# Performance work log

Measured on AMD Instinct MI355X. Metric: run time of the kernel, lower is better.

Reference implementation:

```python
import jax, jax.numpy as jnp
import numpy as np


def conv1x1(x, w, b):
    # x: [B,Cin,H,W], w: [Cout,Cin], b: [Cout]
    return jnp.einsum('bchw,oc->bohw', x, w) + b[None, :, None, None]


def setup_inputs() -> dict:
    key = jax.random.key(0)
    ks = jax.random.split(key, 10)
    B, Cm, C, H, W = 4, 6, 64, 64, 64
    map1 = jax.random.normal(ks[0], (B, Cm, H, W), jnp.float32)
    map2 = jax.random.normal(ks[1], (B, Cm, H, W), jnp.float32)
    feature_map = jax.random.normal(ks[2], (B, C, H, W), jnp.float32)
    # 1x1 conv params (kaiming-ish scale)
    wb = jax.random.normal(ks[3], (Cm, Cm), jnp.float32) / np.sqrt(Cm)
    bb = jnp.zeros((Cm,), jnp.float32)
    wc = jax.random.normal(ks[4], (Cm, Cm), jnp.float32) / np.sqrt(Cm)
    bc = jnp.zeros((Cm,), jnp.float32)
    wd = jax.random.normal(ks[5], (C, C), jnp.float32) / np.sqrt(C)
    bd = jnp.zeros((C,), jnp.float32)
    alpha = jnp.zeros((1,), jnp.float32)
    return {"map1": map1, "map2": map2, "feature_map": feature_map,
            "wb": wb, "bb": bb, "wc": wc, "bc": bc, "wd": wd, "bd": bd,
            "alpha": alpha}


def reference(map1, map2, feature_map, wb, bb, wc, bc, wd, bd, alpha):
    B, _, H, W = map1.shape
    N = H * W
    # conv1x1 projections, flatten spatial
    feat_b = conv1x1(map1, wb, bb).reshape(B, -1, N).transpose(0, 2, 1)  # [B,N,6]
    feat_c = conv1x1(map2, wc, bc).reshape(B, -1, N)                      # [B,6,N]
    attention_s = jax.nn.softmax(jnp.einsum('bnc,bcm->bnm', feat_b, feat_c), axis=-1)  # [B,N,N]
    feat_d = conv1x1(feature_map, wd, bd).reshape(B, -1, N)               # [B,C,N]
    # bmm with attention_s^T: out[b,c,n] = sum_m feat_d[b,c,m] * attn[b,n,m]
    feat_e = jnp.einsum('bcm,bnm->bcn', feat_d, attention_s).reshape(B, -1, H, W)
    return alpha * feat_e + feature_map
```

## Files before the change

kernel.cpp:

```cpp
#include <hip/hip_runtime.h>
#include <hip/hip_bf16.h>
#include <math.h>


#define BATCH 4
#define CMAP  6
#define CH    64
#define NSP   4096
#define TN    64
#define NTH   32
#define PSTR  72

typedef __attribute__((ext_vector_type(8))) short short8;
typedef __attribute__((ext_vector_type(4))) float f32x4;

#if __has_builtin(__builtin_amdgcn_exp2f)
#define EXP2(x) __builtin_amdgcn_exp2f(x)
#else
#define EXP2(x) exp2f(x)
#endif

__device__ __forceinline__ unsigned f2bf(float f) {
    unsigned u = __float_as_uint(f);
    return (u + 0x7fffu + ((u >> 16) & 1u)) >> 16;
}

#define INVLN2 1.44269504088896f
#define SHIFT_BF16 0xC238u
#define ONE_BF16   0x3F80u


__global__ void proj_kernel(const float* __restrict__ map1, const float* __restrict__ map2,
                            const float* __restrict__ fm,
                            const float* __restrict__ wb, const float* __restrict__ bb,
                            const float* __restrict__ wc, const float* __restrict__ bc,
                            const float* __restrict__ wd, const float* __restrict__ bd,
                            unsigned short* __restrict__ featq8,
                            unsigned short* __restrict__ featk8,
                            unsigned short* __restrict__ featdf)
{
    __shared__ unsigned short vfrag[2048];

    const int b    = blockIdx.z;
    const int half = blockIdx.y;
    const int lane = threadIdx.x & 63;
    const int og   = threadIdx.x >> 6;
    const int n    = blockIdx.x * 64 + lane;

    const int ht = lane >> 5;
    const int mm = lane & 31;
    const int q4 = mm >> 3, jj = mm & 7;
    const int cb_local = og >> 1;
    float vals[CH];
#pragma unroll
    for (int c = 0; c < CH; ++c)
        vals[c] = fm[(size_t)(b*CH + c)*NSP + n];
#pragma unroll
    for (int oi = 0; oi < 8; ++oi) {
        const int o = half*32 + og*8 + oi;
        float a = bd[o];
#pragma unroll
        for (int c = 0; c < CH; ++c)
            a = fmaf(vals[c], wd[o*CH + c], a);
        const int r = (og & 1)*8 + oi;
        vfrag[(ht*2 + cb_local)*512 + (q4*16 + r)*8 + jj] = (unsigned short)f2bf(a);
    }

    if (half == 0 && og == 0) {
        float v1[CMAP], v2[CMAP];
#pragma unroll
        for (int c = 0; c < CMAP; ++c) {
            v1[c] = map1[(size_t)(b*CMAP + c)*NSP + n];
            v2[c] = map2[(size_t)(b*CMAP + c)*NSP + n];
        }
        unsigned qv[CMAP], kv[CMAP];
#pragma unroll
        for (int o = 0; o < CMAP; ++o) {
            float a1 = bb[o], a2 = bc[o];
#pragma unroll
            for (int c = 0; c < CMAP; ++c) {
                a1 = fmaf(v1[c], wb[o*CMAP + c], a1);
                a2 = fmaf(v2[c], wc[o*CMAP + c], a2);
            }
            qv[o] = f2bf(a1 * INVLN2);
            kv[o] = f2bf(a2);
        }
        uint4 qw, kw;
        qw.x = qv[0] | (qv[1] << 16);
        qw.y = qv[2] | (qv[3] << 16);
        qw.z = qv[4] | (qv[5] << 16);
        qw.w = SHIFT_BF16;
        kw.x = kv[0] | (kv[1] << 16);
        kw.y = kv[2] | (kv[3] << 16);
        kw.z = kv[4] | (kv[5] << 16);
        kw.w = ONE_BF16;
        *(uint4*)&featq8[(size_t)(b*NSP + n)*8] = qw;
        *(uint4*)&featk8[(size_t)(b*NSP + n)*8] = kw;
    }

    __syncthreads();

    {
        const int tt = threadIdx.x;
        const uint4 d = *(const uint4*)&vfrag[tt*8];
        const int ht2 = tt >> 7, inner = tt & 127;
        const size_t off = (((size_t)(b*128 + blockIdx.x*2 + ht2)*4) + half*2)*512
                         + (size_t)inner*8;
        *(uint4*)&featdf[off] = d;
    }
}

__global__ __launch_bounds__(256, 4)
void attn_kernel(const unsigned short* __restrict__ featq8,
                 const unsigned short* __restrict__ featk8,
                 const unsigned short* __restrict__ featdf,
                 const float* __restrict__ fm, const float* __restrict__ alpha_p,
                 float* __restrict__ out)
{
    __shared__ unsigned short p_scr[2][4][16*PSTR];
    __shared__ float cmb[2][64][20];

    const int b    = blockIdx.z;
    const int chh  = blockIdx.y;
    const int t    = threadIdx.x;
    const int lane = t & 63, w = t >> 6;
    const int row16 = lane & 15, quad = lane >> 4;
    const int qsub  = w >> 1;
    const int khalf = w & 1;
    const int n0w  = blockIdx.x * 32 + qsub * 16;
    const int m0   = khalf * (NSP/2);

    short8 qf = {0,0,0,0,0,0,0,0};
    if (quad == 0)
        qf = *(const short8*)&featq8[(size_t)(b*NSP + n0w + row16)*8];

    const short8 onesb = {(short)ONE_BF16,(short)ONE_BF16,(short)ONE_BF16,(short)ONE_BF16,
                          (short)ONE_BF16,(short)ONE_BF16,(short)ONE_BF16,(short)ONE_BF16};

    const unsigned short* kbase = featk8 + ((size_t)(b*NSP + m0) + row16)*8 + quad*8;
    const unsigned short* vfb = featdf + ((size_t)b*128*4)*512 + lane*8;
    const int hb  = khalf * 64;
    const int cb0 = chh*2, cb1 = chh*2 + 1;

    const f32x4 zf = {0.f,0.f,0.f,0.f};
    f32x4 acc[2] = {zf, zf};
    f32x4 accL = zf;
    const int prow = row16 * PSTR;

#define PAM_DO(pwp, mb, sv)                                                     \
    {                                                                           \
        const float p0 = EXP2(sv[0]), p1 = EXP2(sv[1]);                         \
        const float p2 = EXP2(sv[2]), p3 = EXP2(sv[3]);                         \
        uint2 pp;                                                               \
        pp.x = __builtin_amdgcn_perm(__float_as_uint(p1), __float_as_uint(p0), 0x07060302u); \
        pp.y = __builtin_amdgcn_perm(__float_as_uint(p3), __float_as_uint(p2), 0x07060302u); \
        *(uint2*)((pwp) + (mb)*16) = pp;                                        \
    }

#define LOADK(mt)                                                               \
    kc0 = *(const short8*)(kbase + ((mt)*TN +  0)*8);                           \
    kc1 = *(const short8*)(kbase + ((mt)*TN + 16)*8);                           \
    kc2 = *(const short8*)(kbase + ((mt)*TN + 32)*8);                           \
    kc3 = *(const short8*)(kbase + ((mt)*TN + 48)*8);

#define LOADV(vt)                                                               \
    vv0 = *(const short8*)(vfb + (size_t)((hb + (vt)*2 + 0)*4 + cb0)*512);      \
    vv1 = *(const short8*)(vfb + (size_t)((hb + (vt)*2 + 1)*4 + cb0)*512);      \
    vv2 = *(const short8*)(vfb + (size_t)((hb + (vt)*2 + 0)*4 + cb1)*512);      \
    vv3 = *(const short8*)(vfb + (size_t)((hb + (vt)*2 + 1)*4 + cb1)*512);

#define PV(a0_, a1_)                                                            \
    acc[0] = __builtin_amdgcn_mfma_f32_16x16x32_bf16(a0_, vv0, acc[0], 0, 0, 0); \
    acc[0] = __builtin_amdgcn_mfma_f32_16x16x32_bf16(a1_, vv1, acc[0], 0, 0, 0); \
    acc[1] = __builtin_amdgcn_mfma_f32_16x16x32_bf16(a0_, vv2, acc[1], 0, 0, 0); \
    acc[1] = __builtin_amdgcn_mfma_f32_16x16x32_bf16(a1_, vv3, acc[1], 0, 0, 0); \
    accL   = __builtin_amdgcn_mfma_f32_16x16x32_bf16(a0_, onesb, accL, 0, 0, 0); \
    accL   = __builtin_amdgcn_mfma_f32_16x16x32_bf16(a1_, onesb, accL, 0, 0, 0);

    short8 kc0, kc1, kc2, kc3;
    short8 vv0, vv1, vv2, vv3;
    f32x4 sp0, sp1, sp2, sp3;

    LOADK(0)
    {
        f32x4 a0 = __builtin_amdgcn_mfma_f32_16x16x32_bf16(kc0, qf, zf, 0, 0, 0);
        f32x4 a1 = __builtin_amdgcn_mfma_f32_16x16x32_bf16(kc1, qf, zf, 0, 0, 0);
        f32x4 a2 = __builtin_amdgcn_mfma_f32_16x16x32_bf16(kc2, qf, zf, 0, 0, 0);
        f32x4 a3 = __builtin_amdgcn_mfma_f32_16x16x32_bf16(kc3, qf, zf, 0, 0, 0);
        LOADK(1)
        unsigned short* pw = &p_scr[0][w][prow + quad*4];
        PAM_DO(pw, 0, a0) PAM_DO(pw, 1, a1) PAM_DO(pw, 2, a2) PAM_DO(pw, 3, a3)
    }
    sp0 = __builtin_amdgcn_mfma_f32_16x16x32_bf16(kc0, qf, zf, 0, 0, 0);
    sp1 = __builtin_amdgcn_mfma_f32_16x16x32_bf16(kc1, qf, zf, 0, 0, 0);
    sp2 = __builtin_amdgcn_mfma_f32_16x16x32_bf16(kc2, qf, zf, 0, 0, 0);
    sp3 = __builtin_amdgcn_mfma_f32_16x16x32_bf16(kc3, qf, zf, 0, 0, 0);
    LOADK(2)
    LOADV(0)

#pragma unroll 2
    for (int i = 2; i < NTH; ++i) {
        const f32x4 t0 = __builtin_amdgcn_mfma_f32_16x16x32_bf16(kc0, qf, zf, 0, 0, 0);
        const f32x4 t1 = __builtin_amdgcn_mfma_f32_16x16x32_bf16(kc1, qf, zf, 0, 0, 0);
        const f32x4 t2 = __builtin_amdgcn_mfma_f32_16x16x32_bf16(kc2, qf, zf, 0, 0, 0);
        const f32x4 t3 = __builtin_amdgcn_mfma_f32_16x16x32_bf16(kc3, qf, zf, 0, 0, 0);

        LOADK(i + 1)

        const unsigned short* pr = &p_scr[i & 1][w][prow + quad*8];
        const short8 a0 = *(const short8*)pr;
        const short8 a1 = *(const short8*)(pr + 32);

        {
            unsigned short* pw = &p_scr[(i + 1) & 1][w][prow + quad*4];
            PAM_DO(pw, 0, sp0) PAM_DO(pw, 1, sp1) PAM_DO(pw, 2, sp2) PAM_DO(pw, 3, sp3)
        }

        PV(a0, a1)

        LOADV(i - 1)

        sp0 = t0; sp1 = t1; sp2 = t2; sp3 = t3;
    }

    {
        const unsigned short* pr = &p_scr[0][w][prow + quad*8];
        const short8 a0 = *(const short8*)pr;
        const short8 a1 = *(const short8*)(pr + 32);
        unsigned short* pw = &p_scr[1][w][prow + quad*4];
        PAM_DO(pw, 0, sp0) PAM_DO(pw, 1, sp1) PAM_DO(pw, 2, sp2) PAM_DO(pw, 3, sp3)
        PV(a0, a1)
        LOADV(31)
    }
    {
        const unsigned short* pr = &p_scr[1][w][prow + quad*8];
        const short8 a0 = *(const short8*)pr;
        const short8 a1 = *(const short8*)(pr + 32);
        PV(a0, a1)
    }
#undef PAM_DO
#undef LOADK
#undef LOADV
#undef PV

    if (khalf == 1) {
        float* c = cmb[qsub][lane];
#pragma unroll
        for (int cb = 0; cb < 2; ++cb)
            *(float4*)&c[cb*4] = (float4){acc[cb][0], acc[cb][1], acc[cb][2], acc[cb][3]};
        *(float4*)&c[16] = (float4){accL[0], accL[1], accL[2], accL[3]};
    }
    __syncthreads();
    if (khalf == 0) {
        const float* c = cmb[qsub][lane];
        const float4 lo = *(const float4*)&c[16];
        const float alpha = alpha_p[0];
        const float c0 = alpha / (accL[0] + lo.x + 1e-30f);
        const float c1 = alpha / (accL[1] + lo.y + 1e-30f);
        const float c2 = alpha / (accL[2] + lo.z + 1e-30f);
        const float c3 = alpha / (accL[3] + lo.w + 1e-30f);
#pragma unroll
        for (int cb = 0; cb < 2; ++cb) {
            const float4 po = *(const float4*)&c[cb*4];
            const int ch = chh*32 + cb*16 + row16;
            const size_t base = (size_t)(b*CH + ch)*NSP + n0w + quad*4;
            const float4 f = *(const float4*)&fm[base];
            float4 o;
            o.x = fmaf(c0, acc[cb][0] + po.x, f.x);
            o.y = fmaf(c1, acc[cb][1] + po.y, f.y);
            o.z = fmaf(c2, acc[cb][2] + po.z, f.z);
            o.w = fmaf(c3, acc[cb][3] + po.w, f.w);
            *(float4*)&out[base] = o;
        }
    }
}

extern "C" void kernel_launch(void* const* d_in, const int* in_sizes, int n_in,
                              void* d_out, int out_size, void* d_ws, size_t ws_size,
                              hipStream_t stream)
{
    const float* map1  = (const float*)d_in[0];
    const float* map2  = (const float*)d_in[1];
    const float* fm    = (const float*)d_in[2];
    const float* wb    = (const float*)d_in[3];
    const float* bb    = (const float*)d_in[4];
    const float* wc    = (const float*)d_in[5];
    const float* bc    = (const float*)d_in[6];
    const float* wd    = (const float*)d_in[7];
    const float* bd    = (const float*)d_in[8];
    const float* alpha = (const float*)d_in[9];
    float* out = (float*)d_out;

    unsigned short* featq8 = (unsigned short*)d_ws;
    unsigned short* featk8 = featq8 + (size_t)BATCH*NSP*8;
    unsigned short* featdf = featk8 + (size_t)BATCH*NSP*8;

    proj_kernel<<<dim3(NSP/64, 2, BATCH), 256, 0, stream>>>(
        map1, map2, fm, wb, bb, wc, bc, wd, bd, featq8, featk8, featdf);
    attn_kernel<<<dim3(NSP/32, 2, BATCH), 256, 0, stream>>>(
        featq8, featk8, featdf, fm, alpha, out);
}
```

Baseline: 123.9 us.

## Keep softmax probabilities in registers and compute all 64 channels per block

The attention kernel now computes the transposed score tile, with K rows permuted so that the MFMA output layout matches the B-operand layout of the P·V MFMA. Exponentiated scores are packed straight into registers, which removes the LDS write/read round trip of the probability scratch. Each block now handles all 64 output channels instead of splitting channels across two blocks, so the QK and exp work is no longer duplicated. The cost is more registers (launch bounds drop to 2 blocks per CU), half as many blocks, and scalar rather than vectorised output stores.

```diff
diff --git a/kernel.cpp b/kernel.cpp
--- a/kernel.cpp
+++ b/kernel.cpp
@@ -9,7 +9,6 @@
 #define NSP   4096
 #define TN    64
 #define NTH   32
-#define PSTR  72
 
 typedef __attribute__((ext_vector_type(8))) short short8;
 typedef __attribute__((ext_vector_type(4))) float f32x4;
@@ -110,18 +109,16 @@
     }
 }
 
-__global__ __launch_bounds__(256, 4)
+__global__ __launch_bounds__(256, 2)
 void attn_kernel(const unsigned short* __restrict__ featq8,
                  const unsigned short* __restrict__ featk8,
                  const unsigned short* __restrict__ featdf,
                  const float* __restrict__ fm, const float* __restrict__ alpha_p,
                  float* __restrict__ out)
 {
-    __shared__ unsigned short p_scr[2][4][16*PSTR];
     __shared__ float cmb[2][64][20];
 
-    const int b    = blockIdx.z;
-    const int chh  = blockIdx.y;
+    const int b    = blockIdx.y;
     const int t    = threadIdx.x;
     const int lane = t & 63, w = t >> 6;
     const int row16 = lane & 15, quad = lane >> 4;
@@ -134,143 +131,128 @@
     if (quad == 0)
         qf = *(const short8*)&featq8[(size_t)(b*NSP + n0w + row16)*8];
 
-    const short8 onesb = {(short)ONE_BF16,(short)ONE_BF16,(short)ONE_BF16,(short)ONE_BF16,
+    const short8 onesA = {(short)ONE_BF16,(short)ONE_BF16,(short)ONE_BF16,(short)ONE_BF16,
                           (short)ONE_BF16,(short)ONE_BF16,(short)ONE_BF16,(short)ONE_BF16};
 
-    const unsigned short* kbase = featk8 + ((size_t)(b*NSP + m0) + row16)*8 + quad*8;
+    const int perm16 = ((row16 >> 2) << 3) + (row16 & 3);
+    const unsigned short* kbase = featk8 + ((size_t)(b*NSP + m0) + perm16)*8 + quad*8;
     const unsigned short* vfb = featdf + ((size_t)b*128*4)*512 + lane*8;
-    const int hb  = khalf * 64;
-    const int cb0 = chh*2, cb1 = chh*2 + 1;
+    const int hb = khalf * 64;
 
     const f32x4 zf = {0.f,0.f,0.f,0.f};
-    f32x4 acc[2] = {zf, zf};
+    f32x4 acc[4] = {zf, zf, zf, zf};
     f32x4 accL = zf;
-    const int prow = row16 * PSTR;
-
-#define PAM_DO(pwp, mb, sv)                                                     \
-    {                                                                           \
-        const float p0 = EXP2(sv[0]), p1 = EXP2(sv[1]);                         \
-        const float p2 = EXP2(sv[2]), p3 = EXP2(sv[3]);                         \
-        uint2 pp;                                                               \
-        pp.x = __builtin_amdgcn_perm(__float_as_uint(p1), __float_as_uint(p0), 0x07060302u); \
-        pp.y = __builtin_amdgcn_perm(__float_as_uint(p3), __float_as_uint(p2), 0x07060302u); \
-        *(uint2*)((pwp) + (mb)*16) = pp;                                        \
-    }
 
 #define LOADK(mt)                                                               \
     kc0 = *(const short8*)(kbase + ((mt)*TN +  0)*8);                           \
-    kc1 = *(const short8*)(kbase + ((mt)*TN + 16)*8);                           \
+    kc1 = *(const short8*)(kbase + ((mt)*TN +  4)*8);                           \
     kc2 = *(const short8*)(kbase + ((mt)*TN + 32)*8);                           \
-    kc3 = *(const short8*)(kbase + ((mt)*TN + 48)*8);
+    kc3 = *(const short8*)(kbase + ((mt)*TN + 36)*8);
 
 #define LOADV(vt)                                                               \
-    vv0 = *(const short8*)(vfb + (size_t)((hb + (vt)*2 + 0)*4 + cb0)*512);      \
-    vv1 = *(const short8*)(vfb + (size_t)((hb + (vt)*2 + 1)*4 + cb0)*512);      \
-    vv2 = *(const short8*)(vfb + (size_t)((hb + (vt)*2 + 0)*4 + cb1)*512);      \
-    vv3 = *(const short8*)(vfb + (size_t)((hb + (vt)*2 + 1)*4 + cb1)*512);
-
-#define PV(a0_, a1_)                                                            \
-    acc[0] = __builtin_amdgcn_mfma_f32_16x16x32_bf16(a0_, vv0, acc[0], 0, 0, 0); \
-    acc[0] = __builtin_amdgcn_mfma_f32_16x16x32_bf16(a1_, vv1, acc[0], 0, 0, 0); \
-    acc[1] = __builtin_amdgcn_mfma_f32_16x16x32_bf16(a0_, vv2, acc[1], 0, 0, 0); \
-    acc[1] = __builtin_amdgcn_mfma_f32_16x16x32_bf16(a1_, vv3, acc[1], 0, 0, 0); \
-    accL   = __builtin_amdgcn_mfma_f32_16x16x32_bf16(a0_, onesb, accL, 0, 0, 0); \
-    accL   = __builtin_amdgcn_mfma_f32_16x16x32_bf16(a1_, onesb, accL, 0, 0, 0);
+    vv0 = *(const short8*)(vfb + (size_t)((hb + (vt)*2 + 0)*4 + 0)*512);        \
+    vv1 = *(const short8*)(vfb + (size_t)((hb + (vt)*2 + 1)*4 + 0)*512);        \
+    vv2 = *(const short8*)(vfb + (size_t)((hb + (vt)*2 + 0)*4 + 1)*512);        \
+    vv3 = *(const short8*)(vfb + (size_t)((hb + (vt)*2 + 1)*4 + 1)*512);        \
+    vv4 = *(const short8*)(vfb + (size_t)((hb + (vt)*2 + 0)*4 + 2)*512);        \
+    vv5 = *(const short8*)(vfb + (size_t)((hb + (vt)*2 + 1)*4 + 2)*512);        \
+    vv6 = *(const short8*)(vfb + (size_t)((hb + (vt)*2 + 0)*4 + 3)*512);        \
+    vv7 = *(const short8*)(vfb + (size_t)((hb + (vt)*2 + 1)*4 + 3)*512);
+
+#define SCORES(d0, d1, d2, d3)                                                  \
+    d0 = __builtin_amdgcn_mfma_f32_16x16x32_bf16(kc0, qf, zf, 0, 0, 0);         \
+    d1 = __builtin_amdgcn_mfma_f32_16x16x32_bf16(kc1, qf, zf, 0, 0, 0);         \
+    d2 = __builtin_amdgcn_mfma_f32_16x16x32_bf16(kc2, qf, zf, 0, 0, 0);         \
+    d3 = __builtin_amdgcn_mfma_f32_16x16x32_bf16(kc3, qf, zf, 0, 0, 0);
+
+#define EXPPACK                                                                 \
+    {                                                                           \
+        const float e0 = EXP2(sp0[0]), e1 = EXP2(sp0[1]);                       \
+        const float e2 = EXP2(sp0[2]), e3 = EXP2(sp0[3]);                       \
+        const float e4 = EXP2(sp1[0]), e5 = EXP2(sp1[1]);                       \
+        const float e6 = EXP2(sp1[2]), e7 = EXP2(sp1[3]);                       \
+        const float e8 = EXP2(sp2[0]), e9 = EXP2(sp2[1]);                       \
+        const float ea = EXP2(sp2[2]), eb = EXP2(sp2[3]);                       \
+        const float ec = EXP2(sp3[0]), ed = EXP2(sp3[1]);                       \
+        const float ee = EXP2(sp3[2]), ef = EXP2(sp3[3]);                       \
+        uint4 u0, u1;                                                           \
+        u0.x = __builtin_amdgcn_perm(__float_as_uint(e1), __float_as_uint(e0), 0x07060302u); \
+        u0.y = __builtin_amdgcn_perm(__float_as_uint(e3), __float_as_uint(e2), 0x07060302u); \
+        u0.z = __builtin_amdgcn_perm(__float_as_uint(e5), __float_as_uint(e4), 0x07060302u); \
+        u0.w = __builtin_amdgcn_perm(__float_as_uint(e7), __float_as_uint(e6), 0x07060302u); \
+        u1.x = __builtin_amdgcn_perm(__float_as_uint(e9), __float_as_uint(e8), 0x07060302u); \
+        u1.y = __builtin_amdgcn_perm(__float_as_uint(eb), __float_as_uint(ea), 0x07060302u); \
+        u1.z = __builtin_amdgcn_perm(__float_as_uint(ed), __float_as_uint(ec), 0x07060302u); \
+        u1.w = __builtin_amdgcn_perm(__float_as_uint(ef), __float_as_uint(ee), 0x07060302u); \
+        pb0 = *(short8*)&u0;                                                    \
+        pb1 = *(short8*)&u1;                                                    \
+    }
+
+#define PVALL                                                                   \
+    acc[0] = __builtin_amdgcn_mfma_f32_16x16x32_bf16(vv0, pb0, acc[0], 0, 0, 0); \
+    acc[0] = __builtin_amdgcn_mfma_f32_16x16x32_bf16(vv1, pb1, acc[0], 0, 0, 0); \
+    acc[1] = __builtin_amdgcn_mfma_f32_16x16x32_bf16(vv2, pb0, acc[1], 0, 0, 0); \
+    acc[1] = __builtin_amdgcn_mfma_f32_16x16x32_bf16(vv3, pb1, acc[1], 0, 0, 0); \
+    acc[2] = __builtin_amdgcn_mfma_f32_16x16x32_bf16(vv4, pb0, acc[2], 0, 0, 0); \
+    acc[2] = __builtin_amdgcn_mfma_f32_16x16x32_bf16(vv5, pb1, acc[2], 0, 0, 0); \
+    acc[3] = __builtin_amdgcn_mfma_f32_16x16x32_bf16(vv6, pb0, acc[3], 0, 0, 0); \
+    acc[3] = __builtin_amdgcn_mfma_f32_16x16x32_bf16(vv7, pb1, acc[3], 0, 0, 0); \
+    accL   = __builtin_amdgcn_mfma_f32_16x16x32_bf16(onesA, pb0, accL, 0, 0, 0); \
+    accL   = __builtin_amdgcn_mfma_f32_16x16x32_bf16(onesA, pb1, accL, 0, 0, 0);
 
     short8 kc0, kc1, kc2, kc3;
-    short8 vv0, vv1, vv2, vv3;
+    short8 vv0, vv1, vv2, vv3, vv4, vv5, vv6, vv7;
+    short8 pb0, pb1;
     f32x4 sp0, sp1, sp2, sp3;
 
     LOADK(0)
-    {
-        f32x4 a0 = __builtin_amdgcn_mfma_f32_16x16x32_bf16(kc0, qf, zf, 0, 0, 0);
-        f32x4 a1 = __builtin_amdgcn_mfma_f32_16x16x32_bf16(kc1, qf, zf, 0, 0, 0);
-        f32x4 a2 = __builtin_amdgcn_mfma_f32_16x16x32_bf16(kc2, qf, zf, 0, 0, 0);
-        f32x4 a3 = __builtin_amdgcn_mfma_f32_16x16x32_bf16(kc3, qf, zf, 0, 0, 0);
-        LOADK(1)
-        unsigned short* pw = &p_scr[0][w][prow + quad*4];
-        PAM_DO(pw, 0, a0) PAM_DO(pw, 1, a1) PAM_DO(pw, 2, a2) PAM_DO(pw, 3, a3)
-    }
-    sp0 = __builtin_amdgcn_mfma_f32_16x16x32_bf16(kc0, qf, zf, 0, 0, 0);
-    sp1 = __builtin_amdgcn_mfma_f32_16x16x32_bf16(kc1, qf, zf, 0, 0, 0);
-    sp2 = __builtin_amdgcn_mfma_f32_16x16x32_bf16(kc2, qf, zf, 0, 0, 0);
-    sp3 = __builtin_amdgcn_mfma_f32_16x16x32_bf16(kc3, qf, zf, 0, 0, 0);
-    LOADK(2)
+    SCORES(sp0, sp1, sp2, sp3)
+    LOADK(1)
     LOADV(0)
 
-#pragma unroll 2
-    for (int i = 2; i < NTH; ++i) {
-        const f32x4 t0 = __builtin_amdgcn_mfma_f32_16x16x32_bf16(kc0, qf, zf, 0, 0, 0);
-        const f32x4 t1 = __builtin_amdgcn_mfma_f32_16x16x32_bf16(kc1, qf, zf, 0, 0, 0);
-        const f32x4 t2 = __builtin_amdgcn_mfma_f32_16x16x32_bf16(kc2, qf, zf, 0, 0, 0);
-        const f32x4 t3 = __builtin_amdgcn_mfma_f32_16x16x32_bf16(kc3, qf, zf, 0, 0, 0);
-
+    for (int i = 1; i < NTH; ++i) {
+        f32x4 t0, t1, t2, t3;
+        SCORES(t0, t1, t2, t3)
         LOADK(i + 1)
 
-        const unsigned short* pr = &p_scr[i & 1][w][prow + quad*8];
-        const short8 a0 = *(const short8*)pr;
-        const short8 a1 = *(const short8*)(pr + 32);
-
-        {
-            unsigned short* pw = &p_scr[(i + 1) & 1][w][prow + quad*4];
-            PAM_DO(pw, 0, sp0) PAM_DO(pw, 1, sp1) PAM_DO(pw, 2, sp2) PAM_DO(pw, 3, sp3)
-        }
-
-        PV(a0, a1)
-
-        LOADV(i - 1)
-
+        EXPPACK
+        PVALL
+
+        LOADV(i)
         sp0 = t0; sp1 = t1; sp2 = t2; sp3 = t3;
     }
 
-    {
-        const unsigned short* pr = &p_scr[0][w][prow + quad*8];
-        const short8 a0 = *(const short8*)pr;
-        const short8 a1 = *(const short8*)(pr + 32);
-        unsigned short* pw = &p_scr[1][w][prow + quad*4];
-        PAM_DO(pw, 0, sp0) PAM_DO(pw, 1, sp1) PAM_DO(pw, 2, sp2) PAM_DO(pw, 3, sp3)
-        PV(a0, a1)
-        LOADV(31)
-    }
-    {
-        const unsigned short* pr = &p_scr[1][w][prow + quad*8];
-        const short8 a0 = *(const short8*)pr;
-        const short8 a1 = *(const short8*)(pr + 32);
-        PV(a0, a1)
-    }
-#undef PAM_DO
+    EXPPACK
+    PVALL
 #undef LOADK
 #undef LOADV
-#undef PV
+#undef SCORES
+#undef EXPPACK
+#undef PVALL
 
     if (khalf == 1) {
         float* c = cmb[qsub][lane];
 #pragma unroll
-        for (int cb = 0; cb < 2; ++cb)
+        for (int cb = 0; cb < 4; ++cb)
             *(float4*)&c[cb*4] = (float4){acc[cb][0], acc[cb][1], acc[cb][2], acc[cb][3]};
-        *(float4*)&c[16] = (float4){accL[0], accL[1], accL[2], accL[3]};
+        c[16] = accL[0];
     }
     __syncthreads();
     if (khalf == 0) {
         const float* c = cmb[qsub][lane];
-        const float4 lo = *(const float4*)&c[16];
         const float alpha = alpha_p[0];
-        const float c0 = alpha / (accL[0] + lo.x + 1e-30f);
-        const float c1 = alpha / (accL[1] + lo.y + 1e-30f);
-        const float c2 = alpha / (accL[2] + lo.z + 1e-30f);
-        const float c3 = alpha / (accL[3] + lo.w + 1e-30f);
-#pragma unroll
-        for (int cb = 0; cb < 2; ++cb) {
+        const float cinv = alpha / (accL[0] + c[16] + 1e-30f);
+        const int n = n0w + row16;
+#pragma unroll
+        for (int cb = 0; cb < 4; ++cb) {
             const float4 po = *(const float4*)&c[cb*4];
-            const int ch = chh*32 + cb*16 + row16;
-            const size_t base = (size_t)(b*CH + ch)*NSP + n0w + quad*4;
-            const float4 f = *(const float4*)&fm[base];
-            float4 o;
-            o.x = fmaf(c0, acc[cb][0] + po.x, f.x);
-            o.y = fmaf(c1, acc[cb][1] + po.y, f.y);
-            o.z = fmaf(c2, acc[cb][2] + po.z, f.z);
-            o.w = fmaf(c3, acc[cb][3] + po.w, f.w);
-            *(float4*)&out[base] = o;
+            const float pv[4] = {po.x, po.y, po.z, po.w};
+#pragma unroll
+            for (int r = 0; r < 4; ++r) {
+                const int ch = cb*16 + quad*4 + r;
+                const size_t idx = (size_t)(b*CH + ch)*NSP + n;
+                out[idx] = fmaf(cinv, acc[cb][r] + pv[r], fm[idx]);
+            }
         }
     }
 }
@@ -297,6 +279,6 @@
 
     proj_kernel<<<dim3(NSP/64, 2, BATCH), 256, 0, stream>>>(
         map1, map2, fm, wb, bb, wc, bc, wd, bd, featq8, featk8, featdf);
-    attn_kernel<<<dim3(NSP/32, 2, BATCH), 256, 0, stream>>>(
+    attn_kernel<<<dim3(NSP/32, BATCH), 256, 0, stream>>>(
         featq8, featk8, featdf, fm, alpha, out);
 }
```

New measurement: 119.5 us. 1.04x faster.
